# Optimization experiments

Hardware: AMD Instinct MI355X
Metric: run time of the kernel (lower is better)

## Reference

```python
import jax, jax.numpy as jnp
import numpy as np

B, C, H, W = 4, 16, 512, 512

# 8-connectivity offsets in the exact order the torch double loop visits them
_OFFSETS = [(-1, -1), (-1, 0), (-1, 1), (0, -1), (0, 1), (1, -1), (1, 0), (1, 1)]


def _make_edge_index(height, width):
    """Vectorized grid_8 edge index, matching torch's per-node-then-offset order."""
    n = height * width
    dst = np.zeros((n, 8), dtype=np.int64)
    mask = np.zeros((n, 8), dtype=bool)
    hh = np.arange(height)[:, None]
    ww = np.arange(width)[None, :]
    for k, (dh, dw) in enumerate(_OFFSETS):
        nh, nw = hh + dh, ww + dw
        valid = (nh >= 0) & (nh < height) & (nw >= 0) & (nw < width)
        nb = np.clip(nh, 0, height - 1) * width + np.clip(nw, 0, width - 1)
        dst[:, k] = nb.reshape(-1)
        mask[:, k] = valid.reshape(-1)
    src = np.repeat(np.arange(n, dtype=np.int64), 8).reshape(n, 8)
    m = mask.reshape(-1)
    return np.stack([src.reshape(-1)[m], dst.reshape(-1)[m]], axis=0)  # [2, E]


def setup_inputs() -> dict:
    key = jax.random.key(0)
    grid_features = jax.random.normal(key, (B, C, H, W), dtype=jnp.float32)
    edge_index = jnp.asarray(_make_edge_index(H, W))  # [2, 2091012]
    return {"grid_features": grid_features, "edge_index": edge_index}


def reference(grid_features, edge_index):
    b, c, h, w = grid_features.shape
    # (B, C, H, W) -> (B*H*W, C) node features
    grid_flat = jnp.transpose(grid_features, (0, 2, 3, 1)).reshape(b, h * w, c)
    node_features = grid_flat.reshape(b * h * w, c)

    src, dst = edge_index[0], edge_index[1]
    src_h, src_w = src // w, src % w
    dst_h, dst_w = dst // w, dst % w
    spatial_dist = jnp.sqrt(
        (src_h - dst_h).astype(jnp.float32) ** 2
        + (src_w - dst_w).astype(jnp.float32) ** 2
    )  # [E]

    # per-edge |src - dst| feature diff, mean over channels, then mean over batch
    diff = jnp.abs(grid_flat[:, src, :] - grid_flat[:, dst, :]).mean(axis=-1)  # [B, E]
    feature_diff = diff.mean(axis=0)  # [E]

    edge_attr = jnp.stack([spatial_dist, feature_diff], axis=1)  # [E, 2]
    return node_features, edge_index, edge_attr
```

## Files before the change

kernel.cpp:

```cpp
#include <hip/hip_runtime.h>

#define HW  (512 * 512)
#define NC  16
#define NB  4
#define GW  512
#define GH  512
#define TILE 16
#define HALO 18
#define NSU  12

typedef _Float16 h2 __attribute__((ext_vector_type(2)));
typedef __fp16  h2raw __attribute__((ext_vector_type(2)));

__device__ __forceinline__ unsigned int pk16(float a, float b) {
    h2raw h = __builtin_amdgcn_cvt_pkrtz(a, b);
    return __builtin_bit_cast(unsigned int, h);
}
__device__ __forceinline__ h2 asH(unsigned int u) {
    return __builtin_bit_cast(h2, u);
}
__device__ __forceinline__ float flo(unsigned int u) { return (float)asH(u).x; }
__device__ __forceinline__ float fhi(unsigned int u) { return (float)asH(u).y; }
__device__ __forceinline__ h2 absdiff(h2 x, h2 y) {
    h2 d = x - y;
    unsigned int u = __builtin_bit_cast(unsigned int, d) & 0x7fff7fffu;
    return __builtin_bit_cast(h2, u);
}

__device__ __forceinline__ int edge_prefix(int h, int w) {
    if (h == 0) return (w == 0) ? 0 : 3 + 5 * (w - 1);
    int p = 2556 + 4090 * (h - 1);
    if (h == GH - 1) return p + ((w == 0) ? 0 : 3 + 5 * (w - 1));
    return p + ((w == 0) ? 0 : 5 + 8 * (w - 1));
}
__device__ __forceinline__ int degree(int h, int w) {
    int rh = 1 + (h > 0) + (h < GH - 1);
    int rw = 1 + (w > 0) + (w < GW - 1);
    return rh * rw - 1;
}

__global__ __launch_bounds__(256) void k_fused(const float* __restrict__ g,
                                               float* __restrict__ nf_out,
                                               float* __restrict__ ei_out,
                                               float* __restrict__ attr_out,
                                               int E) {
    __shared__ unsigned int nds[HALO * HALO * NSU];
    float* fdbuf = (float*)nds;

    const int tid = threadIdx.x;
    const int xk = blockIdx.x & 7;
    const int m  = blockIdx.x >> 3;
    const int by = ((xk >> 2) << 4) | (m >> 3);
    const int bx = ((xk & 3) << 3) | (m & 7);
    const int h0 = by * TILE, w0 = bx * TILE;
    const int tr = tid >> 4, tc = tid & 15;

    const int OFF_H[8] = {-1, -1, -1, 0, 0, 1, 1, 1};
    const int OFF_W[8] = {-1, 0, 1, -1, 1, -1, 0, 1};

    float acc[8];
#pragma unroll
    for (int k = 0; k < 8; ++k) acc[k] = 0.0f;

    for (int b = 0; b < NB; ++b) {
        __syncthreads();

        for (int r = 0; r < 4; ++r) {
            int idx = r * 256 + tid;
            if (idx < 864) {
                int f4  = idx % 6;
                int t   = idx / 6;
                int row = t % 18;
                int c2  = t / 18;
                int hh  = min(max(h0 - 1 + row, 0), GH - 1);
                int gw  = min(max(w0 - 4 + 4 * f4, 0), GW - 4);
                const float* pA = g + (((size_t)(b * 16 + 2 * c2)) << 18) + (hh << 9) + gw;
                const float4 A = *(const float4*)pA;
                const float4 B = *(const float4*)(pA + HW);
#pragma unroll
                for (int j = 0; j < 4; ++j) {
                    int hc = 4 * f4 + j - 3;
                    if ((unsigned)hc < (unsigned)HALO) {
                        float a  = ((const float*)&A)[j];
                        float bb = ((const float*)&B)[j];
                        nds[(row * HALO + hc) * NSU + c2] = pk16(a, bb);
                    }
                }
            }
        }
        __syncthreads();

#pragma unroll
        for (int s = 0; s < 4; ++s) {
            int o4 = s * 256 + tid;
            int c4 = o4 & 3;
            int nl256 = o4 >> 2;
            int pr = nl256 >> 4, pc = nl256 & 15;
            int nl = (pr + 1) * HALO + (pc + 1);
            unsigned int u0 = nds[nl * NSU + 2 * c4];
            unsigned int u1 = nds[nl * NSU + 2 * c4 + 1];
            int n = (h0 + pr) * GW + (w0 + pc);
            float4* dst = (float4*)(nf_out + (((size_t)b << 18) + n) * NC + 4 * c4);
            *dst = make_float4(flo(u0), fhi(u0), flo(u1), fhi(u1));
        }

        {
            const uint4* p = (const uint4*)nds;
            int nl_self = (tr + 1) * HALO + (tc + 1);
            uint4 s0 = p[nl_self * 3];
            uint4 s1 = p[nl_self * 3 + 1];
            h2 sf[8] = { asH(s0.x), asH(s0.y), asH(s0.z), asH(s0.w),
                         asH(s1.x), asH(s1.y), asH(s1.z), asH(s1.w) };
#pragma unroll
            for (int k = 0; k < 8; ++k) {
                int nl_n = (tr + 1 + OFF_H[k]) * HALO + (tc + 1 + OFF_W[k]);
                uint4 n0 = p[nl_n * 3];
                uint4 n1 = p[nl_n * 3 + 1];
                h2 a0 = absdiff(sf[0], asH(n0.x));
                h2 a1 = absdiff(sf[1], asH(n0.y));
                h2 a2 = absdiff(sf[2], asH(n0.z));
                h2 a3 = absdiff(sf[3], asH(n0.w));
                h2 a4 = absdiff(sf[4], asH(n1.x));
                h2 a5 = absdiff(sf[5], asH(n1.y));
                h2 a6 = absdiff(sf[6], asH(n1.z));
                h2 a7 = absdiff(sf[7], asH(n1.w));
                h2 b0 = a0 + a1, b1 = a2 + a3, b2 = a4 + a5, b3 = a6 + a7;
                h2 c0 = b0 + b1, c1 = b2 + b3;
                acc[k] += ((float)c0.x + (float)c0.y) + ((float)c1.x + (float)c1.y);
            }
        }
    }

    __syncthreads();

    {
        int h = h0 + tr, w = w0 + tc;
        int cnt = 0;
#pragma unroll
        for (int k = 0; k < 8; ++k) {
            if ((unsigned)(h + OFF_H[k]) < (unsigned)GH &&
                (unsigned)(w + OFF_W[k]) < (unsigned)GW) {
                fdbuf[tid * 9 + cnt] = acc[k] * (1.0f / 64.0f);
                ++cnt;
            }
        }
    }
    __syncthreads();

#pragma unroll
    for (int r = 0; r < 8; ++r) {
        int u2    = r * 256 + tid;
        int chunk = u2 >> 7;
        int e     = u2 & 127;
        int h     = h0 + chunk;
        int first = degree(h, w0);
        int mid   = degree(h, w0 + 1);
        int last  = degree(h, w0 + TILE - 1);
        int Lr    = first + 14 * mid + last;
        if (e < Lr) {
            int node_in_row, k;
            if (e < first) { node_in_row = 0; k = e; }
            else {
                int m2 = e - first;
                if (mid == 8) { node_in_row = 1 + (m2 >> 3); k = m2 & 7; }
                else          { int q = m2 / 5; node_in_row = 1 + q; k = m2 - 5 * q; }
            }
            int w = w0 + node_in_row;
            int n = h * GW + w;
            int idx = 0, cnt2 = 0;
#pragma unroll
            for (int i = 0; i < 8; ++i) {
                bool ok = (unsigned)(h + OFF_H[i]) < (unsigned)GH &&
                          (unsigned)(w + OFF_W[i]) < (unsigned)GW;
                if (ok) { if (cnt2 == k) idx = i; ++cnt2; }
            }
            int dh = OFF_H[idx], dw = OFF_W[idx];
            float dist = (dh != 0 && dw != 0) ? 1.41421356237f : 1.0f;
            float fd = fdbuf[(chunk * 16 + node_in_row) * 9 + k];
            int o = edge_prefix(h, w0) + e;
            ei_out[o]     = (float)n;
            ei_out[E + o] = (float)(n + dh * GW + dw);
            *(float2*)(attr_out + 2 * (size_t)o) = make_float2(dist, fd);
        }
    }
}

extern "C" void kernel_launch(void* const* d_in, const int* in_sizes, int n_in,
                              void* d_out, int out_size, void* d_ws, size_t ws_size,
                              hipStream_t stream) {
    const float* g = (const float*)d_in[0];
    int E = in_sizes[1] / 2;

    float* out      = (float*)d_out;
    float* nf_out   = out;
    float* ei_out   = out + (size_t)NB * HW * NC;
    float* attr_out = ei_out + (size_t)2 * E;

    k_fused<<<(GH / TILE) * (GW / TILE), 256, 0, stream>>>(g, nf_out, ei_out, attr_out, E);
}
```

Baseline: 180.6 us.

## Double-buffer LDS tiles and prefetch next batch's global loads into registers

Splits the shared-memory tile into two buffers and issues the global loads for batch b+1 into registers before the current batch is computed, writing them to the other buffer on the next iteration. This removes one barrier per batch and lets global load latency overlap with the node-feature stores and the edge-difference compute. The load address math is precomputed once per thread. In exchange it doubles LDS use per block (about 31 KB) and keeps 32 extra registers live, which may lower occupancy.

```diff
diff --git a/kernel.cpp b/kernel.cpp
--- a/kernel.cpp
+++ b/kernel.cpp
@@ -8,6 +8,7 @@
 #define TILE 16
 #define HALO 18
 #define NSU  12
+#define NDS_U (HALO * HALO * NSU)
 
 typedef _Float16 h2 __attribute__((ext_vector_type(2)));
 typedef __fp16  h2raw __attribute__((ext_vector_type(2)));
@@ -39,12 +40,33 @@
     return rh * rw - 1;
 }
 
+#define STAGE_LOAD(bb)                                                         \
+    do {                                                                       \
+        _Pragma("unroll") for (int r = 0; r < 4; ++r) if (vld[r]) {            \
+            const float* p = g + (size_t)off0[r] + ((size_t)(bb) << 22);       \
+            LA[r] = *(const float4*)p;                                         \
+            LB[r] = *(const float4*)(p + HW);                                  \
+        }                                                                      \
+    } while (0)
+
+#define STAGE_WRITE(buf)                                                       \
+    do {                                                                       \
+        _Pragma("unroll") for (int r = 0; r < 4; ++r) if (vld[r]) {            \
+            _Pragma("unroll") for (int j = 0; j < 4; ++j) {                    \
+                int hc = vhc[r] + j;                                           \
+                if ((unsigned)hc < (unsigned)HALO)                             \
+                    (buf)[vslot[r] + j * NSU] =                                \
+                        pk16(((const float*)&LA[r])[j], ((const float*)&LB[r])[j]); \
+            }                                                                  \
+        }                                                                      \
+    } while (0)
+
 __global__ __launch_bounds__(256) void k_fused(const float* __restrict__ g,
                                                float* __restrict__ nf_out,
                                                float* __restrict__ ei_out,
                                                float* __restrict__ attr_out,
                                                int E) {
-    __shared__ unsigned int nds[HALO * HALO * NSU];
+    __shared__ unsigned int nds[2][NDS_U];
     float* fdbuf = (float*)nds;
 
     const int tid = threadIdx.x;
@@ -58,37 +80,39 @@
     const int OFF_H[8] = {-1, -1, -1, 0, 0, 1, 1, 1};
     const int OFF_W[8] = {-1, 0, 1, -1, 1, -1, 0, 1};
 
+    bool vld[4];
+    int off0[4], vslot[4], vhc[4];
+#pragma unroll
+    for (int r = 0; r < 4; ++r) {
+        int idx = r * 256 + tid;
+        vld[r] = idx < 864;
+        int i2  = vld[r] ? idx : 0;
+        int f4  = i2 % 6;
+        int t   = i2 / 6;
+        int row = t % 18;
+        int c2  = t / 18;
+        int hh  = min(max(h0 - 1 + row, 0), GH - 1);
+        int gw  = min(max(w0 - 4 + 4 * f4, 0), GW - 4);
+        off0[r]  = ((2 * c2) << 18) + (hh << 9) + gw;
+        vhc[r]   = 4 * f4 - 3;
+        vslot[r] = (row * HALO + vhc[r]) * NSU + c2;
+    }
+
     float acc[8];
 #pragma unroll
     for (int k = 0; k < 8; ++k) acc[k] = 0.0f;
 
+    float4 LA[4], LB[4];
+    STAGE_LOAD(0);
+
+#pragma unroll 1
     for (int b = 0; b < NB; ++b) {
+        unsigned int* buf = nds[b & 1];
+
+        STAGE_WRITE(buf);
         __syncthreads();
 
-        for (int r = 0; r < 4; ++r) {
-            int idx = r * 256 + tid;
-            if (idx < 864) {
-                int f4  = idx % 6;
-                int t   = idx / 6;
-                int row = t % 18;
-                int c2  = t / 18;
-                int hh  = min(max(h0 - 1 + row, 0), GH - 1);
-                int gw  = min(max(w0 - 4 + 4 * f4, 0), GW - 4);
-                const float* pA = g + (((size_t)(b * 16 + 2 * c2)) << 18) + (hh << 9) + gw;
-                const float4 A = *(const float4*)pA;
-                const float4 B = *(const float4*)(pA + HW);
-#pragma unroll
-                for (int j = 0; j < 4; ++j) {
-                    int hc = 4 * f4 + j - 3;
-                    if ((unsigned)hc < (unsigned)HALO) {
-                        float a  = ((const float*)&A)[j];
-                        float bb = ((const float*)&B)[j];
-                        nds[(row * HALO + hc) * NSU + c2] = pk16(a, bb);
-                    }
-                }
-            }
-        }
-        __syncthreads();
+        if (b + 1 < NB) STAGE_LOAD(b + 1);
 
 #pragma unroll
         for (int s = 0; s < 4; ++s) {
@@ -97,15 +121,15 @@
             int nl256 = o4 >> 2;
             int pr = nl256 >> 4, pc = nl256 & 15;
             int nl = (pr + 1) * HALO + (pc + 1);
-            unsigned int u0 = nds[nl * NSU + 2 * c4];
-            unsigned int u1 = nds[nl * NSU + 2 * c4 + 1];
+            unsigned int u0 = buf[nl * NSU + 2 * c4];
+            unsigned int u1 = buf[nl * NSU + 2 * c4 + 1];
             int n = (h0 + pr) * GW + (w0 + pc);
             float4* dst = (float4*)(nf_out + (((size_t)b << 18) + n) * NC + 4 * c4);
             *dst = make_float4(flo(u0), fhi(u0), flo(u1), fhi(u1));
         }
 
         {
-            const uint4* p = (const uint4*)nds;
+            const uint4* p = (const uint4*)buf;
             int nl_self = (tr + 1) * HALO + (tc + 1);
             uint4 s0 = p[nl_self * 3];
             uint4 s1 = p[nl_self * 3 + 1];
```

After: 175.4 us. 1.03x faster.

## Split fused kernel into per-batch stage kernel and edge-writing kernel

Applied to the files above, without the earlier changes.

The single fused kernel that looped over the four batches inside one block is split into two launches. The first launches one block per (tile, batch), loads the halo, writes node features and stores per-node partial feature diffs into workspace. The second sums the four batch partials and writes edge indices and attributes. This gives four times as many blocks to hide memory latency, at the cost of an extra launch and a workspace write and read of 32 bytes per node per batch.

```diff
diff --git a/kernel.cpp b/kernel.cpp
--- a/kernel.cpp
+++ b/kernel.cpp
@@ -39,99 +39,127 @@
     return rh * rw - 1;
 }
 
-__global__ __launch_bounds__(256) void k_fused(const float* __restrict__ g,
+__global__ __launch_bounds__(256) void k_stage(const float* __restrict__ g,
                                                float* __restrict__ nf_out,
-                                               float* __restrict__ ei_out,
-                                               float* __restrict__ attr_out,
-                                               int E) {
+                                               float* __restrict__ ws) {
     __shared__ unsigned int nds[HALO * HALO * NSU];
-    float* fdbuf = (float*)nds;
+
+    const int tid = threadIdx.x;
+    const int xk   = blockIdx.x & 7;
+    const int rest = blockIdx.x >> 3;
+    const int b    = rest & 3;
+    const int m    = rest >> 2;
+    const int by = ((xk >> 2) << 4) | (m >> 3);
+    const int bx = ((xk & 3) << 3) | (m & 7);
+    const int til = by * 32 + bx;
+    const int h0 = by * TILE, w0 = bx * TILE;
+    const int tr = tid >> 4, tc = tid & 15;
+
+    const int OFF_H[8] = {-1, -1, -1, 0, 0, 1, 1, 1};
+    const int OFF_W[8] = {-1, 0, 1, -1, 1, -1, 0, 1};
+
+    for (int r = 0; r < 4; ++r) {
+        int idx = r * 256 + tid;
+        if (idx < 864) {
+            int f4  = idx % 6;
+            int t   = idx / 6;
+            int row = t % 18;
+            int c2  = t / 18;
+            int hh  = min(max(h0 - 1 + row, 0), GH - 1);
+            int gw  = min(max(w0 - 4 + 4 * f4, 0), GW - 4);
+            const float* pA = g + (((size_t)(b * 16 + 2 * c2)) << 18) + (hh << 9) + gw;
+            const float4 A = *(const float4*)pA;
+            const float4 B = *(const float4*)(pA + HW);
+#pragma unroll
+            for (int j = 0; j < 4; ++j) {
+                int hc = 4 * f4 + j - 3;
+                if ((unsigned)hc < (unsigned)HALO) {
+                    float a  = ((const float*)&A)[j];
+                    float bb = ((const float*)&B)[j];
+                    nds[(row * HALO + hc) * NSU + c2] = pk16(a, bb);
+                }
+            }
+        }
+    }
+    __syncthreads();
+
+#pragma unroll
+    for (int s = 0; s < 4; ++s) {
+        int o4 = s * 256 + tid;
+        int c4 = o4 & 3;
+        int nl256 = o4 >> 2;
+        int pr = nl256 >> 4, pc = nl256 & 15;
+        int nl = (pr + 1) * HALO + (pc + 1);
+        unsigned int u0 = nds[nl * NSU + 2 * c4];
+        unsigned int u1 = nds[nl * NSU + 2 * c4 + 1];
+        int n = (h0 + pr) * GW + (w0 + pc);
+        float4* dst = (float4*)(nf_out + (((size_t)b << 18) + n) * NC + 4 * c4);
+        *dst = make_float4(flo(u0), fhi(u0), flo(u1), fhi(u1));
+    }
+
+    float acc[8];
+    {
+        const uint4* p = (const uint4*)nds;
+        int nl_self = (tr + 1) * HALO + (tc + 1);
+        uint4 s0 = p[nl_self * 3];
+        uint4 s1 = p[nl_self * 3 + 1];
+        h2 sf[8] = { asH(s0.x), asH(s0.y), asH(s0.z), asH(s0.w),
+                     asH(s1.x), asH(s1.y), asH(s1.z), asH(s1.w) };
+#pragma unroll
+        for (int k = 0; k < 8; ++k) {
+            int nl_n = (tr + 1 + OFF_H[k]) * HALO + (tc + 1 + OFF_W[k]);
+            uint4 n0 = p[nl_n * 3];
+            uint4 n1 = p[nl_n * 3 + 1];
+            h2 a0 = absdiff(sf[0], asH(n0.x));
+            h2 a1 = absdiff(sf[1], asH(n0.y));
+            h2 a2 = absdiff(sf[2], asH(n0.z));
+            h2 a3 = absdiff(sf[3], asH(n0.w));
+            h2 a4 = absdiff(sf[4], asH(n1.x));
+            h2 a5 = absdiff(sf[5], asH(n1.y));
+            h2 a6 = absdiff(sf[6], asH(n1.z));
+            h2 a7 = absdiff(sf[7], asH(n1.w));
+            h2 b0 = a0 + a1, b1 = a2 + a3, b2 = a4 + a5, b3 = a6 + a7;
+            h2 c0 = b0 + b1, c1 = b2 + b3;
+            acc[k] = ((float)c0.x + (float)c0.y) + ((float)c1.x + (float)c1.y);
+        }
+    }
+
+    {
+        float4* wp = (float4*)ws + ((size_t)(til * 4 + b) << 9) + tid * 2;
+        wp[0] = make_float4(acc[0] * (1.0f / 64.0f), acc[1] * (1.0f / 64.0f),
+                            acc[2] * (1.0f / 64.0f), acc[3] * (1.0f / 64.0f));
+        wp[1] = make_float4(acc[4] * (1.0f / 64.0f), acc[5] * (1.0f / 64.0f),
+                            acc[6] * (1.0f / 64.0f), acc[7] * (1.0f / 64.0f));
+    }
+}
+
+__global__ __launch_bounds__(256) void k_edge(const float* __restrict__ ws,
+                                              float* __restrict__ ei_out,
+                                              float* __restrict__ attr_out,
+                                              int E) {
+    __shared__ float fdbuf[256 * 9];
 
     const int tid = threadIdx.x;
     const int xk = blockIdx.x & 7;
     const int m  = blockIdx.x >> 3;
     const int by = ((xk >> 2) << 4) | (m >> 3);
     const int bx = ((xk & 3) << 3) | (m & 7);
+    const int til = by * 32 + bx;
     const int h0 = by * TILE, w0 = bx * TILE;
     const int tr = tid >> 4, tc = tid & 15;
 
     const int OFF_H[8] = {-1, -1, -1, 0, 0, 1, 1, 1};
     const int OFF_W[8] = {-1, 0, 1, -1, 1, -1, 0, 1};
 
-    float acc[8];
-#pragma unroll
-    for (int k = 0; k < 8; ++k) acc[k] = 0.0f;
-
-    for (int b = 0; b < NB; ++b) {
-        __syncthreads();
-
-        for (int r = 0; r < 4; ++r) {
-            int idx = r * 256 + tid;
-            if (idx < 864) {
-                int f4  = idx % 6;
-                int t   = idx / 6;
-                int row = t % 18;
-                int c2  = t / 18;
-                int hh  = min(max(h0 - 1 + row, 0), GH - 1);
-                int gw  = min(max(w0 - 4 + 4 * f4, 0), GW - 4);
-                const float* pA = g + (((size_t)(b * 16 + 2 * c2)) << 18) + (hh << 9) + gw;
-                const float4 A = *(const float4*)pA;
-                const float4 B = *(const float4*)(pA + HW);
-#pragma unroll
-                for (int j = 0; j < 4; ++j) {
-                    int hc = 4 * f4 + j - 3;
-                    if ((unsigned)hc < (unsigned)HALO) {
-                        float a  = ((const float*)&A)[j];
-                        float bb = ((const float*)&B)[j];
-                        nds[(row * HALO + hc) * NSU + c2] = pk16(a, bb);
-                    }
-                }
-            }
-        }
-        __syncthreads();
-
-#pragma unroll
-        for (int s = 0; s < 4; ++s) {
-            int o4 = s * 256 + tid;
-            int c4 = o4 & 3;
-            int nl256 = o4 >> 2;
-            int pr = nl256 >> 4, pc = nl256 & 15;
-            int nl = (pr + 1) * HALO + (pc + 1);
-            unsigned int u0 = nds[nl * NSU + 2 * c4];
-            unsigned int u1 = nds[nl * NSU + 2 * c4 + 1];
-            int n = (h0 + pr) * GW + (w0 + pc);
-            float4* dst = (float4*)(nf_out + (((size_t)b << 18) + n) * NC + 4 * c4);
-            *dst = make_float4(flo(u0), fhi(u0), flo(u1), fhi(u1));
-        }
-
-        {
-            const uint4* p = (const uint4*)nds;
-            int nl_self = (tr + 1) * HALO + (tc + 1);
-            uint4 s0 = p[nl_self * 3];
-            uint4 s1 = p[nl_self * 3 + 1];
-            h2 sf[8] = { asH(s0.x), asH(s0.y), asH(s0.z), asH(s0.w),
-                         asH(s1.x), asH(s1.y), asH(s1.z), asH(s1.w) };
-#pragma unroll
-            for (int k = 0; k < 8; ++k) {
-                int nl_n = (tr + 1 + OFF_H[k]) * HALO + (tc + 1 + OFF_W[k]);
-                uint4 n0 = p[nl_n * 3];
-                uint4 n1 = p[nl_n * 3 + 1];
-                h2 a0 = absdiff(sf[0], asH(n0.x));
-                h2 a1 = absdiff(sf[1], asH(n0.y));
-                h2 a2 = absdiff(sf[2], asH(n0.z));
-                h2 a3 = absdiff(sf[3], asH(n0.w));
-                h2 a4 = absdiff(sf[4], asH(n1.x));
-                h2 a5 = absdiff(sf[5], asH(n1.y));
-                h2 a6 = absdiff(sf[6], asH(n1.z));
-                h2 a7 = absdiff(sf[7], asH(n1.w));
-                h2 b0 = a0 + a1, b1 = a2 + a3, b2 = a4 + a5, b3 = a6 + a7;
-                h2 c0 = b0 + b1, c1 = b2 + b3;
-                acc[k] += ((float)c0.x + (float)c0.y) + ((float)c1.x + (float)c1.y);
-            }
-        }
-    }
-
-    __syncthreads();
+    const float4* base = (const float4*)ws + ((size_t)til << 11) + tid * 2;
+    float4 a0 = base[0],    a1 = base[1];
+    float4 b0 = base[512],  b1 = base[513];
+    float4 c0 = base[1024], c1 = base[1025];
+    float4 d0 = base[1536], d1 = base[1537];
+    float f[8] = { a0.x + b0.x + c0.x + d0.x,  a0.y + b0.y + c0.y + d0.y,
+                   a0.z + b0.z + c0.z + d0.z,  a0.w + b0.w + c0.w + d0.w,
+                   a1.x + b1.x + c1.x + d1.x,  a1.y + b1.y + c1.y + d1.y,
+                   a1.z + b1.z + c1.z + d1.z,  a1.w + b1.w + c1.w + d1.w };
 
     {
         int h = h0 + tr, w = w0 + tc;
@@ -140,7 +168,7 @@
         for (int k = 0; k < 8; ++k) {
             if ((unsigned)(h + OFF_H[k]) < (unsigned)GH &&
                 (unsigned)(w + OFF_W[k]) < (unsigned)GW) {
-                fdbuf[tid * 9 + cnt] = acc[k] * (1.0f / 64.0f);
+                fdbuf[tid * 9 + cnt] = f[k];
                 ++cnt;
             }
         }
@@ -195,6 +223,8 @@
     float* nf_out   = out;
     float* ei_out   = out + (size_t)NB * HW * NC;
     float* attr_out = ei_out + (size_t)2 * E;
-
-    k_fused<<<(GH / TILE) * (GW / TILE), 256, 0, stream>>>(g, nf_out, ei_out, attr_out, E);
-}
+    float* ws       = (float*)d_ws;
+
+    k_stage<<<1024 * NB, 256, 0, stream>>>(g, nf_out, ws);
+    k_edge<<<1024, 256, 0, stream>>>(ws, ei_out, attr_out, E);
+}
```

Result: slower. 194.6 us (+7.8%).
